# Performance work log

Hardware: AMD Instinct MI355X
Metric: run time of the kernel (lower is better)

The kernel has to match this reference:

```python
import jax, jax.numpy as jnp
import numpy as np

N_HEADS = 32
N_KV_HEADS = 8
THETA = 10000.0


def _rope_tables(head_dim, seq_len):
    # freqs: [head_dim//2]
    freqs = 1.0 / (THETA ** (jnp.arange(0, head_dim, 2, dtype=jnp.float32) / head_dim))
    ang = jnp.arange(seq_len, dtype=jnp.float32)[:, None] * freqs[None, :]  # [T, hd/2]
    return jnp.cos(ang), jnp.sin(ang)


def _apply_rope(x, cos, sin):
    # x: [B, T, H, hd]; cos/sin: [T, hd/2] -> broadcast [1, T, 1, hd/2]
    x_even = x[..., 0::2]
    x_odd = x[..., 1::2]
    c = cos[None, :, None, :]
    s = sin[None, :, None, :]
    out_even = x_even * c - x_odd * s
    out_odd = x_even * s + x_odd * c
    # interleave back to [..., hd]
    out = jnp.stack([out_even, out_odd], axis=-1)
    return out.reshape(x.shape)


def setup_inputs() -> dict:
    key = jax.random.key(0)
    ks = jax.random.split(key, 5)
    B, T, C = 2, 2048, 2048
    kv_dim = (C // N_HEADS) * N_KV_HEADS  # 512
    sc = 1.0 / np.sqrt(C)
    return {
        "x": jax.random.normal(ks[0], (B, T, C), dtype=jnp.float32),
        "wq": jax.random.normal(ks[1], (C, C), dtype=jnp.float32) * sc,
        "wk": jax.random.normal(ks[2], (C, kv_dim), dtype=jnp.float32) * sc,
        "wv": jax.random.normal(ks[3], (C, kv_dim), dtype=jnp.float32) * sc,
        "wo": jax.random.normal(ks[4], (C, C), dtype=jnp.float32) * sc,
    }


def reference(x, wq, wk, wv, wo):
    B, T, C = x.shape
    hd = C // N_HEADS
    rep = N_HEADS // N_KV_HEADS

    q = (x @ wq).reshape(B, T, N_HEADS, hd)
    k = (x @ wk).reshape(B, T, N_KV_HEADS, hd)
    v = (x @ wv).reshape(B, T, N_KV_HEADS, hd)

    cos, sin = _rope_tables(hd, T)
    q = _apply_rope(q, cos, sin)
    k = _apply_rope(k, cos, sin)

    q = q.transpose(0, 2, 1, 3)  # [B, H, T, hd]
    k = k.transpose(0, 2, 1, 3)  # [B, KV, T, hd]
    v = v.transpose(0, 2, 1, 3)

    # GQA: repeat_interleave kv heads to match q heads
    k = jnp.repeat(k, rep, axis=1)
    v = jnp.repeat(v, rep, axis=1)

    scores = jnp.einsum("bhtd,bhsd->bhts", q, k) / jnp.sqrt(jnp.float32(hd))
    weights = jax.nn.softmax(scores, axis=-1)  # no causal mask, as in source
    out = jnp.einsum("bhts,bhsd->bhtd", weights, v)
    out = out.transpose(0, 2, 1, 3).reshape(B, T, C)
    return out @ wo
```

## Files before the change

### kernel.cpp

```cpp
#include <hip/hip_runtime.h>
#include <hip/hip_bf16.h>


typedef unsigned short u16;
typedef short bf16x8 __attribute__((ext_vector_type(8)));
typedef float f32x4 __attribute__((ext_vector_type(4)));
typedef unsigned uint32x4 __attribute__((ext_vector_type(4)));

#define LOG2E 1.4426950408889634f
#define NFREQ (-13.287712379549449f / 32.f)

#if __has_builtin(__builtin_amdgcn_exp2f)
#define EXP2F(x) __builtin_amdgcn_exp2f(x)
#else
#define EXP2F(x) exp2f(x)
#endif

__device__ __forceinline__ float bf2f(u16 u) {
    union { unsigned v; float f; } x; x.v = ((unsigned)u) << 16; return x.f;
}
__device__ __forceinline__ u16 f2bf(float f) {
    unsigned u = __float_as_uint(f);
    u += 0x7fffu + ((u >> 16) & 1u);
    return (u16)(u >> 16);
}
__device__ __forceinline__ unsigned pack_bf16x2(float lo, float hi) {
    unsigned ul = (__float_as_uint(lo) + 0x8000u) >> 16;
    unsigned uh = (__float_as_uint(hi) + 0x8000u) & 0xffff0000u;
    return uh | ul;
}

__device__ __forceinline__ void async_copy16(const void* g, void* l) {
    __builtin_amdgcn_global_load_lds((const __attribute__((address_space(1))) void*)g,
                                     (__attribute__((address_space(3))) void*)l, 16, 0, 0);
}

__global__ void prep_kernel(const float* __restrict__ x,
                            const float* __restrict__ wq, const float* __restrict__ wk,
                            const float* __restrict__ wv, const float* __restrict__ wo,
                            u16* __restrict__ xbf, u16* __restrict__ wqkvT,
                            u16* __restrict__ woT, float2* __restrict__ rtab) {
    const int bz = blockIdx.z;
    if (bz < 4) {
        const int K = 2048;
        const float* W; u16* Wt; int N;
        switch (bz) {
            case 0:  W = wq; Wt = wqkvT;                        N = 2048; break;
            case 1:  W = wk; Wt = wqkvT + (size_t)2048 * 2048;  N = 512;  break;
            case 2:  W = wv; Wt = wqkvT + (size_t)2560 * 2048;  N = 512;  break;
            default: W = wo; Wt = woT;                          N = 2048; break;
        }
        if ((int)blockIdx.x * 32 >= N) return;
        __shared__ float tile[32][33];
        int xx = blockIdx.x * 32 + threadIdx.x;
        int y0 = blockIdx.y * 32 + threadIdx.y;
        #pragma unroll
        for (int r = 0; r < 32; r += 8)
            tile[threadIdx.y + r][threadIdx.x] = W[(size_t)(y0 + r) * N + xx];
        __syncthreads();
        int xo = blockIdx.y * 32 + threadIdx.x;
        int yo0 = blockIdx.x * 32 + threadIdx.y;
        #pragma unroll
        for (int r = 0; r < 32; r += 8)
            Wt[(size_t)(yo0 + r) * K + xo] = f2bf(tile[threadIdx.x][threadIdx.y + r]);
    } else if (bz == 4) {
        int bid = blockIdx.y * gridDim.x + blockIdx.x;
        int tid = threadIdx.y * 32 + threadIdx.x;
        const size_t n4 = (size_t)4096 * 2048 / 4;
        for (size_t i = (size_t)bid * 256 + tid; i < n4; i += (size_t)4096 * 256) {
            float4 v = ((const float4*)x)[i];
            ushort4 o;
            o.x = f2bf(v.x); o.y = f2bf(v.y); o.z = f2bf(v.z); o.w = f2bf(v.w);
            ((ushort4*)xbf)[i] = o;
        }
    } else {
        int bid = blockIdx.y * gridDim.x + blockIdx.x;
        int idx = bid * 256 + threadIdx.y * 32 + threadIdx.x;
        if (idx < 2048 * 32) {
            int t = idx >> 5, i = idx & 31;
            float freq = exp2f((float)i * NFREQ);
            float s, c;
            sincosf((float)t * freq, &s, &c);
            rtab[idx] = make_float2(c, s);
        }
    }
}

__global__ void transpose_perm_kernel(const u16* __restrict__ in, u16* __restrict__ out,
                                      int R, int C) {
    __shared__ u16 tile[32][33];
    int xx = blockIdx.x * 32 + threadIdx.x;
    int y0 = blockIdx.y * 32;
    #pragma unroll
    for (int r = threadIdx.y; r < 32; r += 8)
        tile[r][threadIdx.x] = in[(size_t)(y0 + r) * C + xx];
    __syncthreads();
    int s = y0 + threadIdx.x;
    int c = s & 127;
    int sp = (s & ~127) | (c & 96) | ((c & 12) << 1) | ((c & 16) >> 2) | (c & 3);
    int yo = blockIdx.x * 32;
    #pragma unroll
    for (int r = threadIdx.y; r < 32; r += 8)
        out[(size_t)(yo + r) * R + sp] = tile[threadIdx.x][r];
}

__global__ __launch_bounds__(256) void gemm_qkv_kernel(const u16* __restrict__ A,
                                                       const u16* __restrict__ Bt,
                                                       u16* __restrict__ qout,
                                                       u16* __restrict__ kout,
                                                       u16* __restrict__ vout,
                                                       const float2* __restrict__ rope_tab,
                                                       int K) {
    __shared__ __align__(16) u16 As[128 * 64];
    __shared__ __align__(16) u16 Bs[128 * 64];
    const int tid = threadIdx.x;
    const int m0 = blockIdx.y * 128;
    const int n0 = blockIdx.x * 128;
    const int w = tid >> 6, lane = tid & 63;
    const int quad = lane >> 4, ln = lane & 15;
    const int wr = (w >> 1) * 64, wc = (w & 1) * 64;

    f32x4 acc[4][4];
    #pragma unroll
    for (int i = 0; i < 4; i++)
        #pragma unroll
        for (int j = 0; j < 4; j++) acc[i][j] = (f32x4){0.f, 0.f, 0.f, 0.f};

    for (int kt = 0; kt < K; kt += 64) {
        #pragma unroll
        for (int p = 0; p < 4; p++) {
            int chunk = p * 256 + tid;
            int r = chunk >> 3, cl = chunk & 7;
            int cg = cl ^ (r & 7);
            async_copy16(&A[(size_t)(m0 + r) * K + kt + cg * 8], &As[chunk * 8]);
            async_copy16(&Bt[(size_t)(n0 + r) * K + kt + cg * 8], &Bs[chunk * 8]);
        }
        __syncthreads();
        #pragma unroll
        for (int kk = 0; kk < 2; kk++) {
            bf16x8 a[4], b[4];
            #pragma unroll
            for (int i = 0; i < 4; i++) {
                int r = wr + i * 16 + ln;
                int cl = (kk * 4 + quad) ^ (ln & 7);
                a[i] = *(const bf16x8*)(&As[r * 64 + cl * 8]);
            }
            #pragma unroll
            for (int j = 0; j < 4; j++) {
                int r = wc + j * 16 + ln;
                int cl = (kk * 4 + quad) ^ (ln & 7);
                b[j] = *(const bf16x8*)(&Bs[r * 64 + cl * 8]);
            }
            #pragma unroll
            for (int i = 0; i < 4; i++)
                #pragma unroll
                for (int j = 0; j < 4; j++)
                    acc[i][j] = __builtin_amdgcn_mfma_f32_16x16x32_bf16(a[i], b[j], acc[i][j], 0, 0, 0);
        }
        __syncthreads();
    }

    int nb = n0 + wc;
    u16* dst; int ldc, coff; bool isv = false; float scale = 1.f;
    if (nb < 2048)      { dst = qout; ldc = 2048; coff = 0;    scale = 0.125f * LOG2E; }
    else if (nb < 2560) { dst = kout; ldc = 512;  coff = 2048; }
    else                { dst = vout; ldc = 512;  coff = 2560; isv = true; }

    if (isv) {
        #pragma unroll
        for (int i = 0; i < 4; i++)
            #pragma unroll
            for (int r = 0; r < 4; r++) {
                int row = m0 + wr + i * 16 + quad * 4 + r;
                #pragma unroll
                for (int j = 0; j < 4; j++)
                    dst[(size_t)row * ldc + nb + j * 16 + ln - coff] = f2bf(acc[i][j][r]);
            }
    } else {
        float fsin = (ln & 1) ? 1.f : -1.f;
        int fidx[4];
        #pragma unroll
        for (int j = 0; j < 4; j++)
            fidx[j] = ((nb + j * 16 + ln) & 63) >> 1;
        #pragma unroll
        for (int i = 0; i < 4; i++)
            #pragma unroll
            for (int r = 0; r < 4; r++) {
                int row = m0 + wr + i * 16 + quad * 4 + r;
                const float2* trow = rope_tab + (size_t)(row & 2047) * 32;
                #pragma unroll
                for (int j = 0; j < 4; j++) {
                    float v = acc[i][j][r];
                    float p = __shfl_xor(v, 1, 64);
                    float2 cs = trow[fidx[j]];
                    float rr = (v * cs.x + fsin * p * cs.y) * scale;
                    dst[(size_t)row * ldc + nb + j * 16 + ln - coff] = f2bf(rr);
                }
            }
    }
}

__global__ __launch_bounds__(256) void gemm_bt_kernel(const u16* __restrict__ A,
                                                      const u16* __restrict__ Bt,
                                                      float* __restrict__ C,
                                                      int M, int N, int K) {
    __shared__ __align__(16) u16 As[128 * 64];
    __shared__ __align__(16) u16 Bs[128 * 64];
    const int tid = threadIdx.x;
    const int m0 = blockIdx.y * 128;
    const int n0 = blockIdx.x * 128;
    const int w = tid >> 6, lane = tid & 63;
    const int quad = lane >> 4, ln = lane & 15;
    const int wr = (w >> 1) * 64, wc = (w & 1) * 64;

    f32x4 acc[4][4];
    #pragma unroll
    for (int i = 0; i < 4; i++)
        #pragma unroll
        for (int j = 0; j < 4; j++) acc[i][j] = (f32x4){0.f, 0.f, 0.f, 0.f};

    for (int kt = 0; kt < K; kt += 64) {
        #pragma unroll
        for (int p = 0; p < 4; p++) {
            int chunk = p * 256 + tid;
            int r = chunk >> 3, cl = chunk & 7;
            int cg = cl ^ (r & 7);
            async_copy16(&A[(size_t)(m0 + r) * K + kt + cg * 8], &As[chunk * 8]);
            async_copy16(&Bt[(size_t)(n0 + r) * K + kt + cg * 8], &Bs[chunk * 8]);
        }
        __syncthreads();
        #pragma unroll
        for (int kk = 0; kk < 2; kk++) {
            bf16x8 a[4], b[4];
            #pragma unroll
            for (int i = 0; i < 4; i++) {
                int r = wr + i * 16 + ln;
                int cl = (kk * 4 + quad) ^ (ln & 7);
                a[i] = *(const bf16x8*)(&As[r * 64 + cl * 8]);
            }
            #pragma unroll
            for (int j = 0; j < 4; j++) {
                int r = wc + j * 16 + ln;
                int cl = (kk * 4 + quad) ^ (ln & 7);
                b[j] = *(const bf16x8*)(&Bs[r * 64 + cl * 8]);
            }
            #pragma unroll
            for (int i = 0; i < 4; i++)
                #pragma unroll
                for (int j = 0; j < 4; j++)
                    acc[i][j] = __builtin_amdgcn_mfma_f32_16x16x32_bf16(a[i], b[j], acc[i][j], 0, 0, 0);
        }
        __syncthreads();
    }
    #pragma unroll
    for (int i = 0; i < 4; i++)
        #pragma unroll
        for (int r = 0; r < 4; r++) {
            int row = m0 + wr + i * 16 + quad * 4 + r;
            #pragma unroll
            for (int j = 0; j < 4; j++)
                C[(size_t)row * N + n0 + wc + j * 16 + ln] = acc[i][j][r];
        }
}

__global__ __launch_bounds__(256) void attn_kernel(const u16* __restrict__ qb,
                                                   const u16* __restrict__ kb,
                                                   const u16* __restrict__ vtb,
                                                   u16* __restrict__ ob) {
    const int T = 2048;
    const int CQ = 2048, CKV = 512;
    __shared__ __align__(16) u16 Ks[128 * 64];
    __shared__ __align__(16) u16 Vt[64 * 128];

    const int tid = threadIdx.x;
    const int bh = blockIdx.y;
    const int b = bh >> 5, h = bh & 31, kvh = h >> 2;
    const int t0 = blockIdx.x * 128;
    const u16* qbase = qb + ((size_t)(b * T + t0) * CQ + h * 64);
    const u16* kbase = kb + ((size_t)(b * T) * CKV + kvh * 64);
    const u16* vtbase = vtb + ((size_t)(kvh * 64)) * 4096 + b * 2048;

    const int w = tid >> 6, lane = tid & 63, quad = lane >> 4, ln = lane & 15;

    bf16x8 ones;
    #pragma unroll
    for (int e = 0; e < 8; e++) ones[e] = (short)0x3F80;

    const u16* kp[4]; const u16* vp[4];
    #pragma unroll
    for (int p = 0; p < 4; p++) {
        int chunk = p * 256 + tid;
        int r = chunk >> 3, cl = chunk & 7;
        int cg = cl ^ (r & 7);
        kp[p] = kbase + (size_t)r * CKV + cg * 8;
        int d = chunk >> 4, cl2 = chunk & 15;
        int cg2 = cl2 ^ (d & 7);
        vp[p] = vtbase + (size_t)d * 4096 + cg2 * 8;
    }

    bf16x8 qf[2][2];
    #pragma unroll
    for (int i = 0; i < 2; i++)
        #pragma unroll
        for (int kk = 0; kk < 2; kk++)
            qf[i][kk] = *(const bf16x8*)(&qbase[(size_t)(w * 32 + i * 16 + ln) * CQ + kk * 32 + quad * 8]);

    f32x4 o_acc[2][4];
    f32x4 l_acc[2];
    #pragma unroll
    for (int i = 0; i < 2; i++) {
        l_acc[i] = (f32x4){0.f, 0.f, 0.f, 0.f};
        #pragma unroll
        for (int j = 0; j < 4; j++) o_acc[i][j] = (f32x4){0.f, 0.f, 0.f, 0.f};
    }

    for (int st = 0; st < T; st += 128) {
        #pragma unroll
        for (int p = 0; p < 4; p++) {
            int chunk = p * 256 + tid;
            async_copy16(kp[p], &Ks[chunk * 8]);
            async_copy16(vp[p], &Vt[chunk * 8]);
            kp[p] += 128 * CKV;
            vp[p] += 128;
        }
        __syncthreads();

        f32x4 s_acc[8][2];
        #pragma unroll
        for (int j = 0; j < 8; j++)
            #pragma unroll
            for (int i = 0; i < 2; i++) s_acc[j][i] = (f32x4){0.f, 0.f, 0.f, 0.f};
        #pragma unroll
        for (int kk = 0; kk < 2; kk++) {
            bf16x8 kf[8];
            #pragma unroll
            for (int j = 0; j < 8; j++) {
                int r = j * 16 + ln;
                int cl = (kk * 4 + quad) ^ (ln & 7);
                kf[j] = *(const bf16x8*)(&Ks[r * 64 + cl * 8]);
            }
            __builtin_amdgcn_s_setprio(1);
            #pragma unroll
            for (int j = 0; j < 8; j++)
                #pragma unroll
                for (int i = 0; i < 2; i++)
                    s_acc[j][i] = __builtin_amdgcn_mfma_f32_16x16x32_bf16(kf[j], qf[i][kk], s_acc[j][i], 0, 0, 0);
            __builtin_amdgcn_s_setprio(0);
        }

        bf16x8 pa[2][4];
        #pragma unroll
        for (int i = 0; i < 2; i++)
            #pragma unroll
            for (int c = 0; c < 4; c++) {
                unsigned w0 = pack_bf16x2(EXP2F(s_acc[2 * c][i][0]),     EXP2F(s_acc[2 * c][i][1]));
                unsigned w1 = pack_bf16x2(EXP2F(s_acc[2 * c][i][2]),     EXP2F(s_acc[2 * c][i][3]));
                unsigned w2 = pack_bf16x2(EXP2F(s_acc[2 * c + 1][i][0]), EXP2F(s_acc[2 * c + 1][i][1]));
                unsigned w3 = pack_bf16x2(EXP2F(s_acc[2 * c + 1][i][2]), EXP2F(s_acc[2 * c + 1][i][3]));
                union { uint32x4 u; bf16x8 b; } pu;
                pu.u = (uint32x4){w0, w1, w2, w3};
                pa[i][c] = pu.b;
            }

        #pragma unroll
        for (int c = 0; c < 4; c++) {
            bf16x8 vb[4];
            #pragma unroll
            for (int jd = 0; jd < 4; jd++) {
                int d = jd * 16 + ln;
                int cg = c * 4 + quad;
                int cl = (cg & 8) | ((cg ^ (d & 7)) & 7);
                vb[jd] = *(const bf16x8*)(&Vt[d * 128 + cl * 8]);
            }
            __builtin_amdgcn_s_setprio(1);
            #pragma unroll
            for (int i = 0; i < 2; i++) {
                l_acc[i] = __builtin_amdgcn_mfma_f32_16x16x32_bf16(pa[i][c], ones, l_acc[i], 0, 0, 0);
                #pragma unroll
                for (int jd = 0; jd < 4; jd++)
                    o_acc[i][jd] = __builtin_amdgcn_mfma_f32_16x16x32_bf16(pa[i][c], vb[jd], o_acc[i][jd], 0, 0, 0);
            }
            __builtin_amdgcn_s_setprio(0);
        }
        __syncthreads();
    }

    #pragma unroll
    for (int i = 0; i < 2; i++)
        #pragma unroll
        for (int rr = 0; rr < 4; rr++) {
            float linv = 1.f / l_acc[i][rr];
            int row = w * 32 + i * 16 + quad * 4 + rr;
            #pragma unroll
            for (int jd = 0; jd < 4; jd++) {
                int col = jd * 16 + ln;
                ob[(size_t)(b * T + t0 + row) * CQ + h * 64 + col] = f2bf(o_acc[i][jd][rr] * linv);
            }
        }
}

#define WS_X_BF   ((size_t)0)
#define WS_WQKVT  ((size_t)16777216)
#define WS_WOT    ((size_t)29360128)
#define WS_QBF    ((size_t)37748736)
#define WS_KBF    ((size_t)54525952)
#define WS_VBF    ((size_t)58720256)
#define WS_ABF    ((size_t)62914560)

extern "C" void kernel_launch(void* const* d_in, const int* in_sizes, int n_in,
                              void* d_out, int out_size, void* d_ws, size_t ws_size,
                              hipStream_t stream) {
    const float* x  = (const float*)d_in[0];
    const float* wq = (const float*)d_in[1];
    const float* wk = (const float*)d_in[2];
    const float* wv = (const float*)d_in[3];
    const float* wo = (const float*)d_in[4];
    char* ws = (char*)d_ws;
    u16* xbf   = (u16*)(ws + WS_X_BF);
    u16* wqkvT = (u16*)(ws + WS_WQKVT);
    u16* woT   = (u16*)(ws + WS_WOT);
    u16* qbf   = (u16*)(ws + WS_QBF);
    u16* kbf   = (u16*)(ws + WS_KBF);
    u16* vbf   = (u16*)(ws + WS_VBF);
    u16* vtbf  = (u16*)(ws + WS_X_BF);
    u16* abf   = (u16*)(ws + WS_ABF);
    float2* rtab = (float2*)(ws + WS_ABF);
    float* out = (float*)d_out;

    prep_kernel<<<dim3(64, 64, 6), dim3(32, 8), 0, stream>>>(x, wq, wk, wv, wo,
                                                             xbf, wqkvT, woT, rtab);

    gemm_qkv_kernel<<<dim3(24, 32), 256, 0, stream>>>(xbf, wqkvT, qbf, kbf, vbf, rtab, 2048);

    transpose_perm_kernel<<<dim3(16, 128), dim3(32, 8), 0, stream>>>(vbf, vtbf, 4096, 512);

    attn_kernel<<<dim3(16, 64), 256, 0, stream>>>(qbf, kbf, vtbf, abf);

    gemm_bt_kernel<<<dim3(16, 32), 256, 0, stream>>>(abf, woT, out, 4096, 2048, 2048);
}
```

Baseline: 327.9 us.

## Double-buffer K/V tiles in attention and use hardware bf16 pack conversion

The attention kernel now keeps two LDS buffers for the K and V tiles. It issues the async global-to-LDS copies for the next tile before computing on the current one, so the loads overlap the MFMA work, and only one barrier per iteration remains. The P-to-bf16 packing switches from manual bit arithmetic to the v_cvt_pk_bf16_f32 instruction. The first QK MFMA now starts from a zero accumulator instead of zero-initializing s_acc. LDS use doubles, which may lower occupancy. It is also unclear whether the async copy completes before the single end-of-loop barrier without an explicit vmcnt wait, so there is a possible race.

```diff
diff --git a/kernel.cpp b/kernel.cpp
--- a/kernel.cpp
+++ b/kernel.cpp
@@ -24,10 +24,10 @@
     u += 0x7fffu + ((u >> 16) & 1u);
     return (u16)(u >> 16);
 }
-__device__ __forceinline__ unsigned pack_bf16x2(float lo, float hi) {
-    unsigned ul = (__float_as_uint(lo) + 0x8000u) >> 16;
-    unsigned uh = (__float_as_uint(hi) + 0x8000u) & 0xffff0000u;
-    return uh | ul;
+__device__ __forceinline__ unsigned cvt_pk_bf16(float lo, float hi) {
+    unsigned r;
+    asm("v_cvt_pk_bf16_f32 %0, %1, %2" : "=v"(r) : "v"(lo), "v"(hi));
+    return r;
 }
 
 __device__ __forceinline__ void async_copy16(const void* g, void* l) {
@@ -269,8 +269,8 @@
                                                    u16* __restrict__ ob) {
     const int T = 2048;
     const int CQ = 2048, CKV = 512;
-    __shared__ __align__(16) u16 Ks[128 * 64];
-    __shared__ __align__(16) u16 Vt[64 * 128];
+    __shared__ __align__(16) u16 Ks[2][128 * 64];
+    __shared__ __align__(16) u16 Vt[2][64 * 128];
 
     const int tid = threadIdx.x;
     const int bh = blockIdx.y;
@@ -287,9 +287,11 @@
     for (int e = 0; e < 8; e++) ones[e] = (short)0x3F80;
 
     const u16* kp[4]; const u16* vp[4];
+    int chunks[4];
     #pragma unroll
     for (int p = 0; p < 4; p++) {
         int chunk = p * 256 + tid;
+        chunks[p] = chunk;
         int r = chunk >> 3, cl = chunk & 7;
         int cg = cl ^ (r & 7);
         kp[p] = kbase + (size_t)r * CKV + cg * 8;
@@ -313,50 +315,74 @@
         #pragma unroll
         for (int j = 0; j < 4; j++) o_acc[i][j] = (f32x4){0.f, 0.f, 0.f, 0.f};
     }
-
+    const f32x4 zero4 = (f32x4){0.f, 0.f, 0.f, 0.f};
+
+    #pragma unroll
+    for (int p = 0; p < 4; p++) {
+        async_copy16(kp[p], &Ks[0][chunks[p] * 8]);
+        async_copy16(vp[p], &Vt[0][chunks[p] * 8]);
+        kp[p] += 128 * CKV;
+        vp[p] += 128;
+    }
+    __syncthreads();
+
+    int cur = 0;
     for (int st = 0; st < T; st += 128) {
-        #pragma unroll
-        for (int p = 0; p < 4; p++) {
-            int chunk = p * 256 + tid;
-            async_copy16(kp[p], &Ks[chunk * 8]);
-            async_copy16(vp[p], &Vt[chunk * 8]);
-            kp[p] += 128 * CKV;
-            vp[p] += 128;
-        }
-        __syncthreads();
+        if (st + 128 < T) {
+            #pragma unroll
+            for (int p = 0; p < 4; p++) {
+                async_copy16(kp[p], &Ks[cur ^ 1][chunks[p] * 8]);
+                async_copy16(vp[p], &Vt[cur ^ 1][chunks[p] * 8]);
+                kp[p] += 128 * CKV;
+                vp[p] += 128;
+            }
+        }
+        const u16* KsC = Ks[cur];
+        const u16* VtC = Vt[cur];
 
         f32x4 s_acc[8][2];
-        #pragma unroll
-        for (int j = 0; j < 8; j++)
-            #pragma unroll
-            for (int i = 0; i < 2; i++) s_acc[j][i] = (f32x4){0.f, 0.f, 0.f, 0.f};
-        #pragma unroll
-        for (int kk = 0; kk < 2; kk++) {
+        {
             bf16x8 kf[8];
             #pragma unroll
             for (int j = 0; j < 8; j++) {
                 int r = j * 16 + ln;
-                int cl = (kk * 4 + quad) ^ (ln & 7);
-                kf[j] = *(const bf16x8*)(&Ks[r * 64 + cl * 8]);
+                int cl = quad ^ (ln & 7);
+                kf[j] = *(const bf16x8*)(&KsC[r * 64 + cl * 8]);
             }
             __builtin_amdgcn_s_setprio(1);
             #pragma unroll
             for (int j = 0; j < 8; j++)
                 #pragma unroll
                 for (int i = 0; i < 2; i++)
-                    s_acc[j][i] = __builtin_amdgcn_mfma_f32_16x16x32_bf16(kf[j], qf[i][kk], s_acc[j][i], 0, 0, 0);
+                    s_acc[j][i] = __builtin_amdgcn_mfma_f32_16x16x32_bf16(kf[j], qf[i][0], zero4, 0, 0, 0);
             __builtin_amdgcn_s_setprio(0);
         }
+        {
+            bf16x8 kf[8];
+            #pragma unroll
+            for (int j = 0; j < 8; j++) {
+                int r = j * 16 + ln;
+                int cl = (4 + quad) ^ (ln & 7);
+                kf[j] = *(const bf16x8*)(&KsC[r * 64 + cl * 8]);
+            }
+            __builtin_amdgcn_s_setprio(1);
+            #pragma unroll
+            for (int j = 0; j < 8; j++)
+                #pragma unroll
+                for (int i = 0; i < 2; i++)
+                    s_acc[j][i] = __builtin_amdgcn_mfma_f32_16x16x32_bf16(kf[j], qf[i][1], s_acc[j][i], 0, 0, 0);
+            __builtin_amdgcn_s_setprio(0);
+        }
 
         bf16x8 pa[2][4];
         #pragma unroll
         for (int i = 0; i < 2; i++)
             #pragma unroll
             for (int c = 0; c < 4; c++) {
-                unsigned w0 = pack_bf16x2(EXP2F(s_acc[2 * c][i][0]),     EXP2F(s_acc[2 * c][i][1]));
-                unsigned w1 = pack_bf16x2(EXP2F(s_acc[2 * c][i][2]),     EXP2F(s_acc[2 * c][i][3]));
-                unsigned w2 = pack_bf16x2(EXP2F(s_acc[2 * c + 1][i][0]), EXP2F(s_acc[2 * c + 1][i][1]));
-                unsigned w3 = pack_bf16x2(EXP2F(s_acc[2 * c + 1][i][2]), EXP2F(s_acc[2 * c + 1][i][3]));
+                unsigned w0 = cvt_pk_bf16(EXP2F(s_acc[2 * c][i][0]),     EXP2F(s_acc[2 * c][i][1]));
+                unsigned w1 = cvt_pk_bf16(EXP2F(s_acc[2 * c][i][2]),     EXP2F(s_acc[2 * c][i][3]));
+                unsigned w2 = cvt_pk_bf16(EXP2F(s_acc[2 * c + 1][i][0]), EXP2F(s_acc[2 * c + 1][i][1]));
+                unsigned w3 = cvt_pk_bf16(EXP2F(s_acc[2 * c + 1][i][2]), EXP2F(s_acc[2 * c + 1][i][3]));
                 union { uint32x4 u; bf16x8 b; } pu;
                 pu.u = (uint32x4){w0, w1, w2, w3};
                 pa[i][c] = pu.b;
@@ -370,7 +396,7 @@
                 int d = jd * 16 + ln;
                 int cg = c * 4 + quad;
                 int cl = (cg & 8) | ((cg ^ (d & 7)) & 7);
-                vb[jd] = *(const bf16x8*)(&Vt[d * 128 + cl * 8]);
+                vb[jd] = *(const bf16x8*)(&VtC[d * 128 + cl * 8]);
             }
             __builtin_amdgcn_s_setprio(1);
             #pragma unroll
@@ -382,7 +408,9 @@
             }
             __builtin_amdgcn_s_setprio(0);
         }
-        __syncthreads();
+
+        __syncthreads();
+        cur ^= 1;
     }
 
     #pragma unroll
```

Measured after the change: 313.7 us. 1.05x faster.
